# Kernel tuning notes

Measured on AMD Instinct MI355X. Metric: run time of the kernel, lower is better.

## Reference

```python
import jax, jax.numpy as jnp
import numpy as np

B, S, DM, H = 2, 2048, 1024, 16
D = DM // H  # head dim = 64


def setup_inputs() -> dict:
    key = jax.random.key(0)
    k1, k2, k3, k4, k5 = jax.random.split(key, 5)
    hidden_states = jax.random.normal(k1, (B, S, DM), dtype=jnp.float32)
    attention_mask = jnp.zeros((B, 1, S, S), dtype=jnp.float32)
    position_ids = jnp.broadcast_to(jnp.arange(S, dtype=jnp.int32), (B, S))
    # nn.Linear weights stored as (out, in); x @ W.T
    Wq = jax.random.normal(k2, (DM, DM), dtype=jnp.float32) * 0.02
    Wk = jax.random.normal(k3, (DM, DM), dtype=jnp.float32) * 0.02
    Wv = jax.random.normal(k4, (DM, DM), dtype=jnp.float32) * 0.02
    return {"hidden_states": hidden_states, "attention_mask": attention_mask,
            "position_ids": position_ids, "Wq": Wq, "Wk": Wk, "Wv": Wv}


def _rotate_half(x):
    h = x.shape[-1] // 2
    return jnp.concatenate((-x[..., h:], x[..., :h]), axis=-1)


def _rope_cos_sin(position_ids, dtype):
    # inv_freq: (D/2,)
    inv_freq = 1.0 / (10000.0 ** (jnp.arange(0, D, 2, dtype=jnp.float32) / D))
    # freqs: (B, S, D/2)
    freqs = position_ids.astype(jnp.float32)[:, :, None] * inv_freq[None, None, :]
    emb = jnp.concatenate((freqs, freqs), axis=-1)  # (B, S, D)
    return jnp.cos(emb).astype(dtype), jnp.sin(emb).astype(dtype)


def reference(hidden_states, attention_mask, position_ids, Wq, Wk, Wv):
    def split_heads(x):  # (B,S,DM) -> (B,H,S,D)
        return x.reshape(B, S, H, D).transpose(0, 2, 1, 3)

    q = split_heads(hidden_states @ Wq.T)
    k = split_heads(hidden_states @ Wk.T)
    v = split_heads(hidden_states @ Wv.T)

    q = q * (D ** -0.5)

    cos, sin = _rope_cos_sin(position_ids, q.dtype)
    cos = cos[:, None, :, :]  # unsqueeze head dim -> (B,1,S,D)
    sin = sin[:, None, :, :]
    q = q * cos + _rotate_half(q) * sin
    k = k * cos + _rotate_half(k) * sin

    # (B,H,S,S)
    scores = jnp.einsum('bhqd,bhkd->bhqk', q, k) + attention_mask
    probs = jax.nn.softmax(scores.astype(jnp.float32), axis=-1).astype(q.dtype)
    ctx = jnp.einsum('bhqk,bhkd->bhqd', probs, v)  # (B,H,S,D)
    ctx = ctx.transpose(0, 2, 1, 3).reshape(B, S, DM)
    return ctx
```

## Files before the change

### kernel.cpp

```cpp
#include <hip/hip_runtime.h>
#include <math.h>

#define B  2
#define S  2048
#define DM 1024
#define H  16
#define Dh 64
#define BH (B*H)

typedef short  bf16x8 __attribute__((ext_vector_type(8)));
typedef float  f32x4  __attribute__((ext_vector_type(4)));

__device__ __forceinline__ unsigned short f2bf(float f) {
    unsigned u = __float_as_uint(f);
    u = (u + 0x7fffu + ((u >> 16) & 1u)) >> 16;
    return (unsigned short)u;
}

__device__ __forceinline__ unsigned cvt_pk_bf16(float lo, float hi) {
    unsigned r;
    asm("v_cvt_pk_bf16_f32 %0, %1, %2" : "=v"(r) : "v"(lo), "v"(hi));
    return r;
}

__global__ __launch_bounds__(256) void cast_kernel(const float* __restrict__ X,
                                                   const float* __restrict__ Wq,
                                                   const float* __restrict__ Wk,
                                                   const float* __restrict__ Wv,
                                                   unsigned short* __restrict__ Xb,
                                                   unsigned short* __restrict__ Wb) {
    const long c = (long)(blockIdx.x * 256 + threadIdx.x) * 4;
    const float* src;
    unsigned short* dst;
    if (c < 4194304L) {
        src = X + c;  dst = Xb + c;
    } else {
        const long c2 = c - 4194304L;
        const int  wi = (int)(c2 >> 20);
        const long r  = c2 & 1048575L;
        src = (wi == 0 ? Wq : (wi == 1 ? Wk : Wv)) + r;
        dst = Wb + c2;
    }
    const float4 v = *(const float4*)src;
    ushort4 o;
    o.x = f2bf(v.x); o.y = f2bf(v.y); o.z = f2bf(v.z); o.w = f2bf(v.w);
    *(ushort4*)dst = o;
}

__global__ __launch_bounds__(256) void rope_tab_kernel(const int* __restrict__ pos,
                                                       float* __restrict__ Tab) {
    const int idx = blockIdx.x * 256 + threadIdx.x;
    const int i  = idx & 31;
    const int bs = idx >> 5;
    const float p   = (float)pos[bs];
    const float inv = exp2f(-(float)i * 0.41524101186092029f);
    float sn, cs;
    sincosf(p * inv, &sn, &cs);
    ((float2*)Tab)[idx] = make_float2(cs, sn);
}

__device__ __forceinline__ void gload_lds16(const unsigned short* g, unsigned short* l) {
    __builtin_amdgcn_global_load_lds(
        (const __attribute__((address_space(1))) unsigned int*)g,
        (__attribute__((address_space(3))) unsigned int*)l,
        16, 0, 0);
}

__global__ __launch_bounds__(256) void qkv_gemm(const unsigned short* __restrict__ Xb,
                                                const unsigned short* __restrict__ Wb,
                                                const float* __restrict__ Tab,
                                                unsigned short* __restrict__ Qb,
                                                unsigned short* __restrict__ Kb,
                                                unsigned short* __restrict__ Vb) {
    __shared__ __align__(16) unsigned short As[128 * 32];
    __shared__ __align__(16) unsigned short Bs[128 * 32];
    __shared__ __align__(16) unsigned short Es[64 * 136];

    const int tid  = threadIdx.x;
    const int w    = tid >> 6;
    const int lane = tid & 63;
    const int col  = lane & 15;
    const int quad = lane >> 4;
    const int m0 = blockIdx.x * 128;
    const int n0 = blockIdx.y * 128;
    const int mw = (w & 1) * 64;
    const int nw = (w >> 1) * 64;

    const int srow = lane >> 2;
    const int sk8  = (((lane & 3) ^ (srow & 3))) * 8;

    f32x4 acc[4][4] = {};

    for (int k0 = 0; k0 < 1024; k0 += 32) {
        __syncthreads();
        #pragma unroll
        for (int it = 0; it < 2; ++it) {
            const int rbase = w * 16 + it * 64;
            gload_lds16(Xb + (size_t)(m0 + rbase + srow) * 1024 + k0 + sk8,
                        &As[rbase * 32]);
            gload_lds16(Wb + (size_t)(n0 + rbase + srow) * 1024 + k0 + sk8,
                        &Bs[rbase * 32]);
        }
        __syncthreads();

        const int fs = (quad ^ (col & 3)) * 8;
        bf16x8 a[4], bb[4];
        #pragma unroll
        for (int i = 0; i < 4; ++i)
            a[i] = *(const bf16x8*)&As[(mw + i * 16 + col) * 32 + fs];
        #pragma unroll
        for (int j = 0; j < 4; ++j)
            bb[j] = *(const bf16x8*)&Bs[(nw + j * 16 + col) * 32 + fs];
        #pragma unroll
        for (int i = 0; i < 4; ++i)
            #pragma unroll
            for (int j = 0; j < 4; ++j)
                acc[i][j] = __builtin_amdgcn_mfma_f32_16x16x32_bf16(a[i], bb[j], acc[i][j], 0, 0, 0);
    }

    const int wsel = n0 >> 10;
    const int hh0  = (n0 & 1023) >> 6;
    const int bb2  = m0 >> 11;
    const int ssb  = m0 & 2047;

    if (wsel == 2) {
        #pragma unroll
        for (int half = 0; half < 2; ++half) {
            __syncthreads();
            if ((w >> 1) == half) {
                #pragma unroll
                for (int i = 0; i < 4; ++i) {
                    const int sl = mw + i * 16 + quad * 4;
                    #pragma unroll
                    for (int j = 0; j < 4; ++j) {
                        const int dl = j * 16 + col;
                        ushort4 ov;
                        ov.x = f2bf(acc[i][j][0]); ov.y = f2bf(acc[i][j][1]);
                        ov.z = f2bf(acc[i][j][2]); ov.w = f2bf(acc[i][j][3]);
                        *(ushort4*)&Es[dl * 136 + sl] = ov;
                    }
                }
            }
            __syncthreads();
            #pragma unroll
            for (int k = 0; k < 4; ++k) {
                const int c  = tid + k * 256;
                const int dl = c >> 4;
                const int s8 = (c & 15) * 8;
                const int d  = half * 64 + dl;
                const bf16x8 v = *(const bf16x8*)&Es[dl * 136 + s8];
                *(bf16x8*)(Vb + ((size_t)(bb2 * H + hh0 + (d >> 6)) * Dh + (d & 63)) * S
                           + ssb + s8) = v;
            }
        }
    } else {
        unsigned short* dp = (wsel == 0) ? Qb : Kb;
        const float qscale = (wsel == 0) ? 0.125f : 1.0f;
        #pragma unroll
        for (int half = 0; half < 2; ++half) {
            __syncthreads();
            if ((w & 1) == half) {
                #pragma unroll
                for (int i = 0; i < 4; ++i) {
                    #pragma unroll
                    for (int r = 0; r < 4; ++r) {
                        const int rl = i * 16 + quad * 4 + r;
                        const int ss = ssb + half * 64 + rl;
                        const float2 t0 = ((const float2*)Tab)[(size_t)(bb2 * S + ss) * 32 + col];
                        const float2 t1 = ((const float2*)Tab)[(size_t)(bb2 * S + ss) * 32 + col + 16];
                        const float a0 = acc[i][0][r] * qscale, a1 = acc[i][1][r] * qscale;
                        const float a2 = acc[i][2][r] * qscale, a3 = acc[i][3][r] * qscale;
                        unsigned short* e = &Es[rl * 136 + nw];
                        e[col]      = f2bf(a0 * t0.x - a2 * t0.y);
                        e[col + 16] = f2bf(a1 * t1.x - a3 * t1.y);
                        e[col + 32] = f2bf(a2 * t0.x + a0 * t0.y);
                        e[col + 48] = f2bf(a3 * t1.x + a1 * t1.y);
                    }
                }
            }
            __syncthreads();
            #pragma unroll
            for (int k = 0; k < 4; ++k) {
                const int c  = tid + k * 256;
                const int rl = c >> 4;
                const int d8 = (c & 15) * 8;
                const bf16x8 v = *(const bf16x8*)&Es[rl * 136 + d8];
                *(bf16x8*)(dp + ((size_t)(bb2 * H + hh0 + (d8 >> 6)) * S
                                 + ssb + half * 64 + rl) * Dh + (d8 & 63)) = v;
            }
        }
    }
}

#define KSd 72
#define LOG2E  1.4426950408889634f
#define NEG8L (-11.541560327111707f)
#define NT (S / 64)

__global__ __launch_bounds__(256) void attn_kernel(const unsigned short* __restrict__ Q,
                                                   const unsigned short* __restrict__ K,
                                                   const unsigned short* __restrict__ V,
                                                   const float* __restrict__ mask,
                                                   float* __restrict__ out) {
    __shared__ __align__(16) unsigned short Ks[2][64 * KSd];
    __shared__ __align__(16) unsigned short Vt[2][64 * KSd];
    __shared__ __align__(16) unsigned short Ps[4 * 32 * KSd];

    const int tid  = threadIdx.x;
    const int w    = tid >> 6;
    const int lane = tid & 63;
    const int col  = lane & 15;
    const int quad = lane >> 4;
    const int bh   = blockIdx.y;
    const int b    = bh >> 4, h = bh & 15;
    const int q0   = blockIdx.x * 128;
    const int qw   = q0 + w * 32;

    const int srow = tid >> 3;
    const int sc8  = (tid & 7) * 8;

    bf16x8 qa[2][2];
    #pragma unroll
    for (int u = 0; u < 2; ++u) {
        const unsigned short* qrow = Q + ((size_t)bh * S + qw + u * 16 + col) * Dh;
        qa[u][0] = *(const bf16x8*)(qrow + quad * 8);
        qa[u][1] = *(const bf16x8*)(qrow + 32 + quad * 8);
    }

    f32x4 o[4][2] = {};
    float lsum[2] = {0.f, 0.f};
    const float* mbase = mask + (size_t)b * S * S;
    unsigned short* pw = Ps + w * 32 * KSd;
    const unsigned short* Kbase = K + (size_t)bh * S * Dh;
    const unsigned short* Vbase = V + (size_t)bh * Dh * S;

    bf16x8 kp[2], vp[2];
    float4 mv[4][2];
    #pragma unroll
    for (int cc = 0; cc < 2; ++cc) {
        kp[cc] = *(const bf16x8*)(Kbase + (size_t)(srow + cc * 32) * Dh + sc8);
        vp[cc] = *(const bf16x8*)(Vbase + (size_t)(srow + cc * 32) * S + sc8);
    }
    #pragma unroll
    for (int u = 0; u < 2; ++u)
        #pragma unroll
        for (int f = 0; f < 4; ++f)
            mv[f][u] = *(const float4*)(mbase + (size_t)(qw + u * 16 + col) * S
                                        + f * 16 + quad * 4);
    #pragma unroll
    for (int cc = 0; cc < 2; ++cc) {
        const int row = srow + cc * 32;
        *(bf16x8*)&Ks[0][row * KSd + sc8] = kp[cc];
        *(bf16x8*)&Vt[0][row * KSd + sc8] = vp[cc];
    }
    __syncthreads();

    for (int kt = 0; kt < NT; ++kt) {
        const int cur = kt & 1;

        float4 mvp[4][2];
        if (kt + 1 < NT) {
            #pragma unroll
            for (int cc = 0; cc < 2; ++cc) {
                kp[cc] = *(const bf16x8*)(Kbase + (size_t)((kt + 1) * 64 + srow + cc * 32) * Dh + sc8);
                vp[cc] = *(const bf16x8*)(Vbase + (size_t)(srow + cc * 32) * S + (kt + 1) * 64 + sc8);
            }
            #pragma unroll
            for (int u = 0; u < 2; ++u)
                #pragma unroll
                for (int f = 0; f < 4; ++f)
                    mvp[f][u] = *(const float4*)(mbase + (size_t)(qw + u * 16 + col) * S
                                                 + (kt + 1) * 64 + f * 16 + quad * 4);
        }

        f32x4 sc[4][2] = {};
        #pragma unroll
        for (int f = 0; f < 4; ++f) {
            const bf16x8 ka0 = *(const bf16x8*)&Ks[cur][(f * 16 + col) * KSd + quad * 8];
            const bf16x8 ka1 = *(const bf16x8*)&Ks[cur][(f * 16 + col) * KSd + 32 + quad * 8];
            #pragma unroll
            for (int u = 0; u < 2; ++u) {
                sc[f][u] = __builtin_amdgcn_mfma_f32_16x16x32_bf16(ka0, qa[u][0], sc[f][u], 0, 0, 0);
                sc[f][u] = __builtin_amdgcn_mfma_f32_16x16x32_bf16(ka1, qa[u][1], sc[f][u], 0, 0, 0);
            }
        }

        #pragma unroll
        for (int u = 0; u < 2; ++u) {
            #pragma unroll
            for (int f = 0; f < 4; ++f) {
                sc[f][u][0] += mv[f][u].x; sc[f][u][1] += mv[f][u].y;
                sc[f][u][2] += mv[f][u].z; sc[f][u][3] += mv[f][u].w;
            }
            #pragma unroll
            for (int f = 0; f < 4; ++f)
                #pragma unroll
                for (int r = 0; r < 4; ++r) {
                    const float pv = __builtin_amdgcn_exp2f(
                        __builtin_fmaf(sc[f][u][r], LOG2E, NEG8L));
                    sc[f][u][r] = pv;
                    lsum[u] += pv;
                }
            unsigned short* pq = pw + (u * 16 + col) * KSd;
            #pragma unroll
            for (int f = 0; f < 4; ++f) {
                *(uint2*)&pq[f * 16 + quad * 4] =
                    make_uint2(cvt_pk_bf16(sc[f][u][0], sc[f][u][1]),
                               cvt_pk_bf16(sc[f][u][2], sc[f][u][3]));
            }
        }

        if (kt + 1 < NT) {
            #pragma unroll
            for (int u = 0; u < 2; ++u)
                #pragma unroll
                for (int f = 0; f < 4; ++f)
                    mv[f][u] = mvp[f][u];
            const int nxt = cur ^ 1;
            #pragma unroll
            for (int cc = 0; cc < 2; ++cc) {
                const int row = srow + cc * 32;
                *(bf16x8*)&Ks[nxt][row * KSd + sc8] = kp[cc];
                *(bf16x8*)&Vt[nxt][row * KSd + sc8] = vp[cc];
            }
        }
        __threadfence_block();

        #pragma unroll
        for (int kc = 0; kc < 2; ++kc) {
            bf16x8 pb[2];
            #pragma unroll
            for (int u = 0; u < 2; ++u)
                pb[u] = *(const bf16x8*)&pw[(u * 16 + col) * KSd + kc * 32 + quad * 8];
            #pragma unroll
            for (int g = 0; g < 4; ++g) {
                const bf16x8 va = *(const bf16x8*)&Vt[cur][(g * 16 + col) * KSd + kc * 32 + quad * 8];
                #pragma unroll
                for (int u = 0; u < 2; ++u)
                    o[g][u] = __builtin_amdgcn_mfma_f32_16x16x32_bf16(va, pb[u], o[g][u], 0, 0, 0);
            }
        }
        __syncthreads();
    }

    #pragma unroll
    for (int u = 0; u < 2; ++u) {
        lsum[u] += __shfl_xor(lsum[u], 16, 64);
        lsum[u] += __shfl_xor(lsum[u], 32, 64);
    }

    #pragma unroll
    for (int u = 0; u < 2; ++u) {
        const float inv = 1.f / lsum[u];
        float* op = out + ((size_t)b * S + qw + u * 16 + col) * DM + h * Dh + quad * 4;
        #pragma unroll
        for (int g = 0; g < 4; ++g) {
            float4 ov;
            ov.x = o[g][u][0] * inv; ov.y = o[g][u][1] * inv;
            ov.z = o[g][u][2] * inv; ov.w = o[g][u][3] * inv;
            *(float4*)(op + g * 16) = ov;
        }
    }
}

extern "C" void kernel_launch(void* const* d_in, const int* in_sizes, int n_in,
                              void* d_out, int out_size, void* d_ws, size_t ws_size,
                              hipStream_t stream) {
    const float* hs   = (const float*)d_in[0];
    const float* mask = (const float*)d_in[1];
    const int*   pos  = (const int*)  d_in[2];
    const float* Wq   = (const float*)d_in[3];
    const float* Wk   = (const float*)d_in[4];
    const float* Wv   = (const float*)d_in[5];
    float* out = (float*)d_out;

    unsigned short* Xb = (unsigned short*)d_ws;
    unsigned short* Wb = Xb + 4194304;
    unsigned short* Qb = Wb + 3145728;
    unsigned short* Kb = Qb + 4194304;
    unsigned short* Vb = Kb + 4194304;
    float*          Tab = (float*)(Vb + 4194304);

    cast_kernel<<<7168, 256, 0, stream>>>(hs, Wq, Wk, Wv, Xb, Wb);
    rope_tab_kernel<<<512, 256, 0, stream>>>(pos, Tab);
    qkv_gemm<<<dim3(32, 24), 256, 0, stream>>>(Xb, Wb, Tab, Qb, Kb, Vb);
    attn_kernel<<<dim3(S / 128, BH), 256, 0, stream>>>(Qb, Kb, Vb, mask, out);
}
```

Measured before the change: 225.3 us.

## Load K/V MFMA fragments directly from global into registers, drop LDS staging

The attention kernel stops staging K and V tiles through double-buffered shared memory with block-wide barriers. Each wave now loads its MFMA operand fragments for K and V straight from global memory into registers and prefetches the next tile's fragments right after use. Launch bounds now request two blocks per CU. The intent is to remove LDS traffic and __syncthreads stalls. In exchange, each wave redundantly fetches the full K/V tile from global/L2 (four times per block) and holds more registers, and the fragment loads are less coalesced.

Measured after the change: 313.3 us. 39.1% more time.

```diff
diff --git a/kernel.cpp b/kernel.cpp
--- a/kernel.cpp
+++ b/kernel.cpp
@@ -197,13 +197,11 @@
 #define NEG8L (-11.541560327111707f)
 #define NT (S / 64)
 
-__global__ __launch_bounds__(256) void attn_kernel(const unsigned short* __restrict__ Q,
-                                                   const unsigned short* __restrict__ K,
-                                                   const unsigned short* __restrict__ V,
-                                                   const float* __restrict__ mask,
-                                                   float* __restrict__ out) {
-    __shared__ __align__(16) unsigned short Ks[2][64 * KSd];
-    __shared__ __align__(16) unsigned short Vt[2][64 * KSd];
+__global__ __launch_bounds__(256, 2) void attn_kernel(const unsigned short* __restrict__ Q,
+                                                      const unsigned short* __restrict__ K,
+                                                      const unsigned short* __restrict__ V,
+                                                      const float* __restrict__ mask,
+                                                      float* __restrict__ out) {
     __shared__ __align__(16) unsigned short Ps[4 * 32 * KSd];
 
     const int tid  = threadIdx.x;
@@ -216,9 +214,6 @@
     const int q0   = blockIdx.x * 128;
     const int qw   = q0 + w * 32;
 
-    const int srow = tid >> 3;
-    const int sc8  = (tid & 7) * 8;
-
     bf16x8 qa[2][2];
     #pragma unroll
     for (int u = 0; u < 2; ++u) {
@@ -231,67 +226,68 @@
     float lsum[2] = {0.f, 0.f};
     const float* mbase = mask + (size_t)b * S * S;
     unsigned short* pw = Ps + w * 32 * KSd;
-    const unsigned short* Kbase = K + (size_t)bh * S * Dh;
-    const unsigned short* Vbase = V + (size_t)bh * Dh * S;
-
-    bf16x8 kp[2], vp[2];
+
+    const unsigned short* Kl = K + (size_t)bh * S * Dh + (size_t)col * Dh + quad * 8;
+    const unsigned short* Vl = V + (size_t)bh * Dh * S + (size_t)col * S + quad * 8;
+
+    bf16x8 kf[4][2], vf[4][2];
     float4 mv[4][2];
-    #pragma unroll
-    for (int cc = 0; cc < 2; ++cc) {
-        kp[cc] = *(const bf16x8*)(Kbase + (size_t)(srow + cc * 32) * Dh + sc8);
-        vp[cc] = *(const bf16x8*)(Vbase + (size_t)(srow + cc * 32) * S + sc8);
-    }
+
+    #pragma unroll
+    for (int f = 0; f < 4; ++f)
+        #pragma unroll
+        for (int kc = 0; kc < 2; ++kc)
+            kf[f][kc] = *(const bf16x8*)(Kl + (size_t)(f * 16) * Dh + kc * 32);
+    #pragma unroll
+    for (int g = 0; g < 4; ++g)
+        #pragma unroll
+        for (int kc = 0; kc < 2; ++kc)
+            vf[g][kc] = *(const bf16x8*)(Vl + (size_t)(g * 16) * S + kc * 32);
     #pragma unroll
     for (int u = 0; u < 2; ++u)
         #pragma unroll
         for (int f = 0; f < 4; ++f)
             mv[f][u] = *(const float4*)(mbase + (size_t)(qw + u * 16 + col) * S
                                         + f * 16 + quad * 4);
-    #pragma unroll
-    for (int cc = 0; cc < 2; ++cc) {
-        const int row = srow + cc * 32;
-        *(bf16x8*)&Ks[0][row * KSd + sc8] = kp[cc];
-        *(bf16x8*)&Vt[0][row * KSd + sc8] = vp[cc];
-    }
-    __syncthreads();
 
     for (int kt = 0; kt < NT; ++kt) {
-        const int cur = kt & 1;
-
-        float4 mvp[4][2];
+        f32x4 sc[4][2] = {};
+        #pragma unroll
+        for (int f = 0; f < 4; ++f)
+            #pragma unroll
+            for (int u = 0; u < 2; ++u) {
+                sc[f][u] = __builtin_amdgcn_mfma_f32_16x16x32_bf16(kf[f][0], qa[u][0], sc[f][u], 0, 0, 0);
+                sc[f][u] = __builtin_amdgcn_mfma_f32_16x16x32_bf16(kf[f][1], qa[u][1], sc[f][u], 0, 0, 0);
+            }
+
         if (kt + 1 < NT) {
-            #pragma unroll
-            for (int cc = 0; cc < 2; ++cc) {
-                kp[cc] = *(const bf16x8*)(Kbase + (size_t)((kt + 1) * 64 + srow + cc * 32) * Dh + sc8);
-                vp[cc] = *(const bf16x8*)(Vbase + (size_t)(srow + cc * 32) * S + (kt + 1) * 64 + sc8);
-            }
-            #pragma unroll
-            for (int u = 0; u < 2; ++u)
-                #pragma unroll
-                for (int f = 0; f < 4; ++f)
-                    mvp[f][u] = *(const float4*)(mbase + (size_t)(qw + u * 16 + col) * S
-                                                 + (kt + 1) * 64 + f * 16 + quad * 4);
-        }
-
-        f32x4 sc[4][2] = {};
-        #pragma unroll
-        for (int f = 0; f < 4; ++f) {
-            const bf16x8 ka0 = *(const bf16x8*)&Ks[cur][(f * 16 + col) * KSd + quad * 8];
-            const bf16x8 ka1 = *(const bf16x8*)&Ks[cur][(f * 16 + col) * KSd + 32 + quad * 8];
-            #pragma unroll
-            for (int u = 0; u < 2; ++u) {
-                sc[f][u] = __builtin_amdgcn_mfma_f32_16x16x32_bf16(ka0, qa[u][0], sc[f][u], 0, 0, 0);
-                sc[f][u] = __builtin_amdgcn_mfma_f32_16x16x32_bf16(ka1, qa[u][1], sc[f][u], 0, 0, 0);
-            }
-        }
-
-        #pragma unroll
-        for (int u = 0; u < 2; ++u) {
+            const unsigned short* kp = Kl + (size_t)(kt + 1) * 64 * Dh;
+            #pragma unroll
+            for (int f = 0; f < 4; ++f)
+                #pragma unroll
+                for (int kc = 0; kc < 2; ++kc)
+                    kf[f][kc] = *(const bf16x8*)(kp + (size_t)(f * 16) * Dh + kc * 32);
+        }
+
+        #pragma unroll
+        for (int u = 0; u < 2; ++u)
             #pragma unroll
             for (int f = 0; f < 4; ++f) {
                 sc[f][u][0] += mv[f][u].x; sc[f][u][1] += mv[f][u].y;
                 sc[f][u][2] += mv[f][u].z; sc[f][u][3] += mv[f][u].w;
             }
+
+        if (kt + 1 < NT) {
+            #pragma unroll
+            for (int u = 0; u < 2; ++u)
+                #pragma unroll
+                for (int f = 0; f < 4; ++f)
+                    mv[f][u] = *(const float4*)(mbase + (size_t)(qw + u * 16 + col) * S
+                                                + (kt + 1) * 64 + f * 16 + quad * 4);
+        }
+
+        #pragma unroll
+        for (int u = 0; u < 2; ++u) {
             #pragma unroll
             for (int f = 0; f < 4; ++f)
                 #pragma unroll
@@ -310,21 +306,8 @@
             }
         }
 
-        if (kt + 1 < NT) {
-            #pragma unroll
-            for (int u = 0; u < 2; ++u)
-                #pragma unroll
-                for (int f = 0; f < 4; ++f)
-                    mv[f][u] = mvp[f][u];
-            const int nxt = cur ^ 1;
-            #pragma unroll
-            for (int cc = 0; cc < 2; ++cc) {
-                const int row = srow + cc * 32;
-                *(bf16x8*)&Ks[nxt][row * KSd + sc8] = kp[cc];
-                *(bf16x8*)&Vt[nxt][row * KSd + sc8] = vp[cc];
-            }
-        }
-        __threadfence_block();
+        asm volatile("s_waitcnt lgkmcnt(0)" ::: "memory");
+        __builtin_amdgcn_sched_barrier(0);
 
         #pragma unroll
         for (int kc = 0; kc < 2; ++kc) {
@@ -333,14 +316,20 @@
             for (int u = 0; u < 2; ++u)
                 pb[u] = *(const bf16x8*)&pw[(u * 16 + col) * KSd + kc * 32 + quad * 8];
             #pragma unroll
-            for (int g = 0; g < 4; ++g) {
-                const bf16x8 va = *(const bf16x8*)&Vt[cur][(g * 16 + col) * KSd + kc * 32 + quad * 8];
+            for (int g = 0; g < 4; ++g)
                 #pragma unroll
                 for (int u = 0; u < 2; ++u)
-                    o[g][u] = __builtin_amdgcn_mfma_f32_16x16x32_bf16(va, pb[u], o[g][u], 0, 0, 0);
-            }
-        }
-        __syncthreads();
+                    o[g][u] = __builtin_amdgcn_mfma_f32_16x16x32_bf16(vf[g][kc], pb[u], o[g][u], 0, 0, 0);
+        }
+
+        if (kt + 1 < NT) {
+            const unsigned short* vp = Vl + (size_t)(kt + 1) * 64;
+            #pragma unroll
+            for (int g = 0; g < 4; ++g)
+                #pragma unroll
+                for (int kc = 0; kc < 2; ++kc)
+                    vf[g][kc] = *(const bf16x8*)(vp + (size_t)(g * 16) * S + kc * 32);
+        }
     }
 
     #pragma unroll
```
